# Optimization experiments

Measured on AMD Instinct MI355X. Metric: run time of the kernel, lower is better.

## Reference

```python
import jax, jax.numpy as jnp
import numpy as np

B, S, D = 2, 2048, 1024
N_EXP, TOP_K = 8, 2
CAP_FACTOR = 1.25

def setup_inputs() -> dict:
    key = jax.random.key(0)
    k1, k2 = jax.random.split(key)
    x = jax.random.normal(k1, (B, S, D), dtype=jnp.float32)
    W_gate = jax.random.normal(k2, (N_EXP, D), dtype=jnp.float32) * (1.0 / np.sqrt(D))
    return {"x": x, "W_gate": W_gate}

def reference(x, W_gate):
    Bq, Sq, d = x.shape
    N = Bq * Sq                      # num_tokens
    n_exp = W_gate.shape[0]
    top_k = TOP_K
    cap = int(N * top_k * CAP_FACTOR / n_exp)  # exp_capacity (static)

    x_flat = x.reshape(N, d)
    logits = x_flat @ W_gate.T                      # [N, n_exp]
    top_vals, top_idx = jax.lax.top_k(logits, top_k)  # [N, k]
    gates = jax.nn.softmax(top_vals, axis=-1)       # [N, k]

    # Serial token-major, k-minor assignment order == flatten row-major.
    e_flat = top_idx.reshape(-1)                    # [N*k]
    oh = jax.nn.one_hot(e_flat, n_exp, dtype=jnp.int32)
    # position within expert = # earlier slots routed to same expert
    pos = (jnp.cumsum(oh, axis=0) - oh)[jnp.arange(N * top_k), e_flat]
    pos_safe = jnp.where(pos < cap, pos, cap)       # cap -> out-of-bounds -> dropped

    tok = jnp.arange(N * top_k) // top_k            # owning token per slot
    g_flat = gates.reshape(-1)

    exp_mask = jnp.zeros((N, n_exp, cap), jnp.float32)
    exp_mask = exp_mask.at[tok, e_flat, pos_safe].set(g_flat, mode='drop')

    exp_batches = jnp.zeros((n_exp, cap, d), jnp.float32)
    exp_batches = exp_batches.at[e_flat, pos_safe].set(x_flat[tok], mode='drop')

    return gates, exp_mask, exp_batches
```

## Files before the change

### kernel.cpp

```cpp
#include <hip/hip_runtime.h>
#include <math.h>

#define NTOK   4096
#define DIM    1024
#define NEXP   8
#define CAP    1280
#define MROW   (NEXP * CAP)

#define OUT_MASK_OFF   ((size_t)NTOK*2)
#define OUT_BATCH_OFF  (OUT_MASK_OFF + (size_t)NTOK*NEXP*CAP)

typedef float f4 __attribute__((ext_vector_type(4)));

__global__ __launch_bounds__(256) void gate_kernel(
    const float* __restrict__ x, const float* __restrict__ Wg,
    float* __restrict__ gates_out,
    int* __restrict__ e0a, int* __restrict__ e1a,
    float* __restrict__ g0a, float* __restrict__ g1a)
{
    const int wave = threadIdx.x >> 6;
    const int lane = threadIdx.x & 63;
    const int t    = blockIdx.x * 4 + wave;

    const f4* xr = (const f4*)(x + (size_t)t * DIM);
    f4 xv[4];
#pragma unroll
    for (int p = 0; p < 4; ++p) xv[p] = xr[p * 64 + lane];

    float acc[NEXP];
#pragma unroll
    for (int e = 0; e < NEXP; ++e) {
        const f4* wr = (const f4*)(Wg + (size_t)e * DIM);
        float a = 0.f;
#pragma unroll
        for (int p = 0; p < 4; ++p) {
            const f4 w = wr[p * 64 + lane];
            a += xv[p].x * w.x + xv[p].y * w.y + xv[p].z * w.z + xv[p].w * w.w;
        }
        acc[e] = a;
    }

#pragma unroll
    for (int off = 32; off >= 1; off >>= 1) {
#pragma unroll
        for (int e = 0; e < NEXP; ++e)
            acc[e] += __shfl_xor(acc[e], off);
    }

    if (lane == 0) {
        float best = -INFINITY, second = -INFINITY;
        int b0 = 0, b1 = 0;
#pragma unroll
        for (int e = 0; e < NEXP; ++e) {
            const float v = acc[e];
            if (v > best)        { second = best; b1 = b0; best = v; b0 = e; }
            else if (v > second) { second = v; b1 = e; }
        }
        const float e1v = __expf(second - best);
        const float inv = 1.0f / (1.0f + e1v);
        const float g0 = inv, g1 = e1v * inv;

        gates_out[(size_t)t * 2]     = g0;
        gates_out[(size_t)t * 2 + 1] = g1;
        e0a[t] = b0; e1a[t] = b1;
        g0a[t] = g0; g1a[t] = g1;
    }
}

__global__ __launch_bounds__(256) void scan_kernel(
    const int* __restrict__ e0a, const int* __restrict__ e1a,
    int* __restrict__ pos0a, int* __restrict__ pos1a,
    int* __restrict__ inv_out)
{
    __shared__ int invs[NEXP * CAP];
    __shared__ unsigned wtot[4][4];

    const int tid  = threadIdx.x;
    const int wave = tid >> 6;
    const int lane = tid & 63;

    for (int i = tid; i < NEXP * CAP; i += 256) invs[i] = -1;

    const int tok0 = tid * 16;
    int ea[16], eb[16];
    {
        const int4* va = (const int4*)(e0a + tok0);
        const int4* vb = (const int4*)(e1a + tok0);
#pragma unroll
        for (int q = 0; q < 4; ++q) {
            int4 a = va[q], b = vb[q];
            ea[4*q] = a.x; ea[4*q+1] = a.y; ea[4*q+2] = a.z; ea[4*q+3] = a.w;
            eb[4*q] = b.x; eb[4*q+1] = b.y; eb[4*q+2] = b.z; eb[4*q+3] = b.w;
        }
    }

    int local[NEXP];
#pragma unroll
    for (int e = 0; e < NEXP; ++e) local[e] = 0;
#pragma unroll
    for (int j = 0; j < 16; ++j) { local[ea[j]]++; local[eb[j]]++; }

    unsigned pk[4];
#pragma unroll
    for (int q = 0; q < 4; ++q)
        pk[q] = (unsigned)local[2*q] | ((unsigned)local[2*q+1] << 16);
    const unsigned my0 = pk[0], my1 = pk[1], my2 = pk[2], my3 = pk[3];

#pragma unroll
    for (int off = 1; off < 64; off <<= 1) {
        unsigned n0 = __shfl_up((int)pk[0], off);
        unsigned n1 = __shfl_up((int)pk[1], off);
        unsigned n2 = __shfl_up((int)pk[2], off);
        unsigned n3 = __shfl_up((int)pk[3], off);
        if (lane >= off) { pk[0] += n0; pk[1] += n1; pk[2] += n2; pk[3] += n3; }
    }

    if (lane == 63) {
#pragma unroll
        for (int q = 0; q < 4; ++q) wtot[wave][q] = pk[q];
    }
    __syncthreads();

#pragma unroll
    for (int w = 0; w < 4; ++w) {
        if (w < wave) {
            pk[0] += wtot[w][0]; pk[1] += wtot[w][1];
            pk[2] += wtot[w][2]; pk[3] += wtot[w][3];
        }
    }
    pk[0] -= my0; pk[1] -= my1; pk[2] -= my2; pk[3] -= my3;

    int run[NEXP];
#pragma unroll
    for (int q = 0; q < 4; ++q) {
        run[2*q]   = (int)(pk[q] & 0xFFFFu);
        run[2*q+1] = (int)(pk[q] >> 16);
    }

    int p0r[16], p1r[16];
#pragma unroll
    for (int j = 0; j < 16; ++j) {
        const int tok = tok0 + j;
        int e = ea[j];
        int p = run[e]++;
        p0r[j] = p;
        if (p < CAP) invs[e * CAP + p] = tok;
        e = eb[j];
        p = run[e]++;
        p1r[j] = p;
        if (p < CAP) invs[e * CAP + p] = tok;
    }

#pragma unroll
    for (int q = 0; q < 4; ++q) {
        ((int4*)(pos0a + tok0))[q] = make_int4(p0r[4*q], p0r[4*q+1], p0r[4*q+2], p0r[4*q+3]);
        ((int4*)(pos1a + tok0))[q] = make_int4(p1r[4*q], p1r[4*q+1], p1r[4*q+2], p1r[4*q+3]);
    }
    __syncthreads();

    for (int i = tid; i < NEXP * CAP / 4; i += 256)
        ((int4*)inv_out)[i] = ((const int4*)invs)[i];
}

#define BATCH_BLOCKS 2560
#define TOTAL_BLOCKS (BATCH_BLOCKS + NTOK)
__global__ __launch_bounds__(256) void writer_kernel(
    const int* __restrict__ e0a, const int* __restrict__ e1a,
    const int* __restrict__ pos0a, const int* __restrict__ pos1a,
    const float* __restrict__ g0a, const float* __restrict__ g1a,
    const int* __restrict__ inv, const float* __restrict__ x,
    float* __restrict__ mask_out, float* __restrict__ batch_out)
{
    const int tid = threadIdx.x;

    if (blockIdx.x < BATCH_BLOCKS) {
        const int4 tk = ((const int4*)inv)[blockIdx.x];
        const int toks[4] = { tk.x, tk.y, tk.z, tk.w };
        const int base = blockIdx.x * 4;
#pragma unroll
        for (int i = 0; i < 4; ++i) {
            const int tok = toks[i];
            f4 v = (f4)(0.f);
            if (tok >= 0)
                v = ((const f4*)(x + (size_t)tok * DIM))[tid];
            __builtin_nontemporal_store(v, (f4*)(batch_out + (size_t)(base + i) * DIM) + tid);
        }
    } else {
        const int t  = blockIdx.x - BATCH_BLOCKS;
        const int e0 = e0a[t], e1 = e1a[t];
        const int p0 = pos0a[t], p1 = pos1a[t];
        const float g0 = g0a[t], g1 = g1a[t];

        const int o0 = e0 * CAP + p0;
        const int o1 = e1 * CAP + p1;
        const int q0 = (p0 < CAP) ? (o0 >> 2) : -1;
        const int c0 = o0 & 3;
        const int q1 = (p1 < CAP) ? (o1 >> 2) : -1;
        const int c1 = o1 & 3;

        f4* row = (f4*)(mask_out + (size_t)t * MROW);
#pragma unroll
        for (int it = 0; it < MROW / 1024; ++it) {
            const int f4i = it * 256 + tid;
            f4 v = (f4)(0.f);
            if (f4i == q0) {
                v.x = (c0 == 0) ? g0 : 0.f;
                v.y = (c0 == 1) ? g0 : 0.f;
                v.z = (c0 == 2) ? g0 : 0.f;
                v.w = (c0 == 3) ? g0 : 0.f;
            }
            if (f4i == q1) {
                v.x = (c1 == 0) ? g1 : v.x;
                v.y = (c1 == 1) ? g1 : v.y;
                v.z = (c1 == 2) ? g1 : v.z;
                v.w = (c1 == 3) ? g1 : v.w;
            }
            __builtin_nontemporal_store(v, row + f4i);
        }
    }
}

extern "C" void kernel_launch(void* const* d_in, const int* in_sizes, int n_in,
                              void* d_out, int out_size, void* d_ws, size_t ws_size,
                              hipStream_t stream)
{
    const float* x  = (const float*)d_in[0];
    const float* Wg = (const float*)d_in[1];

    float* out   = (float*)d_out;
    float* gates = out;
    float* mask  = out + OUT_MASK_OFF;
    float* batch = out + OUT_BATCH_OFF;

    int* wsi = (int*)d_ws;
    int*   e0a  = wsi;
    int*   e1a  = wsi + NTOK;
    float* g0a  = (float*)(wsi + 2 * NTOK);
    float* g1a  = (float*)(wsi + 3 * NTOK);
    int*   p0a  = wsi + 4 * NTOK;
    int*   p1a  = wsi + 5 * NTOK;
    int*   inv  = wsi + 6 * NTOK;

    gate_kernel  <<<NTOK / 4, 256, 0, stream>>>(x, Wg, gates, e0a, e1a, g0a, g1a);
    scan_kernel  <<<1, 256, 0, stream>>>(e0a, e1a, p0a, p1a, inv);
    writer_kernel<<<TOTAL_BLOCKS, 256, 0, stream>>>(
        e0a, e1a, p0a, p1a, g0a, g1a, inv, x, mask, batch);
}
```

Measured before the change: 239.3 us.

## Fuse gate, scan and writer kernels into one cooperative kernel with grid syncs

```diff
diff --git a/kernel.cpp b/kernel.cpp
--- a/kernel.cpp
+++ b/kernel.cpp
@@ -1,5 +1,8 @@
 #include <hip/hip_runtime.h>
+#include <hip/hip_cooperative_groups.h>
 #include <math.h>
+
+namespace cg = cooperative_groups;
 
 #define NTOK   4096
 #define DIM    1024
@@ -10,212 +13,210 @@
 #define OUT_MASK_OFF   ((size_t)NTOK*2)
 #define OUT_BATCH_OFF  (OUT_MASK_OFF + (size_t)NTOK*NEXP*CAP)
 
+#define GRID_BLKS    1024
+#define BATCH_GROUPS 2560
+#define TOTAL_UNITS  (NTOK + BATCH_GROUPS)
+
 typedef float f4 __attribute__((ext_vector_type(4)));
 
-__global__ __launch_bounds__(256) void gate_kernel(
+__global__ __launch_bounds__(256) void moe_fused(
     const float* __restrict__ x, const float* __restrict__ Wg,
     float* __restrict__ gates_out,
+    float* __restrict__ mask_out, float* __restrict__ batch_out,
     int* __restrict__ e0a, int* __restrict__ e1a,
-    float* __restrict__ g0a, float* __restrict__ g1a)
+    float* __restrict__ g0a, float* __restrict__ g1a,
+    int* __restrict__ pos0a, int* __restrict__ pos1a,
+    int* __restrict__ inv)
 {
-    const int wave = threadIdx.x >> 6;
-    const int lane = threadIdx.x & 63;
-    const int t    = blockIdx.x * 4 + wave;
-
-    const f4* xr = (const f4*)(x + (size_t)t * DIM);
-    f4 xv[4];
-#pragma unroll
-    for (int p = 0; p < 4; ++p) xv[p] = xr[p * 64 + lane];
-
-    float acc[NEXP];
-#pragma unroll
-    for (int e = 0; e < NEXP; ++e) {
-        const f4* wr = (const f4*)(Wg + (size_t)e * DIM);
-        float a = 0.f;
-#pragma unroll
-        for (int p = 0; p < 4; ++p) {
-            const f4 w = wr[p * 64 + lane];
-            a += xv[p].x * w.x + xv[p].y * w.y + xv[p].z * w.z + xv[p].w * w.w;
-        }
-        acc[e] = a;
-    }
-
-#pragma unroll
-    for (int off = 32; off >= 1; off >>= 1) {
-#pragma unroll
-        for (int e = 0; e < NEXP; ++e)
-            acc[e] += __shfl_xor(acc[e], off);
-    }
-
-    if (lane == 0) {
-        float best = -INFINITY, second = -INFINITY;
-        int b0 = 0, b1 = 0;
-#pragma unroll
-        for (int e = 0; e < NEXP; ++e) {
-            const float v = acc[e];
-            if (v > best)        { second = best; b1 = b0; best = v; b0 = e; }
-            else if (v > second) { second = v; b1 = e; }
-        }
-        const float e1v = __expf(second - best);
-        const float inv = 1.0f / (1.0f + e1v);
-        const float g0 = inv, g1 = e1v * inv;
-
-        gates_out[(size_t)t * 2]     = g0;
-        gates_out[(size_t)t * 2 + 1] = g1;
-        e0a[t] = b0; e1a[t] = b1;
-        g0a[t] = g0; g1a[t] = g1;
-    }
-}
-
-__global__ __launch_bounds__(256) void scan_kernel(
-    const int* __restrict__ e0a, const int* __restrict__ e1a,
-    int* __restrict__ pos0a, int* __restrict__ pos1a,
-    int* __restrict__ inv_out)
-{
-    __shared__ int invs[NEXP * CAP];
-    __shared__ unsigned wtot[4][4];
+    cg::grid_group grid = cg::this_grid();
 
     const int tid  = threadIdx.x;
     const int wave = tid >> 6;
     const int lane = tid & 63;
 
-    for (int i = tid; i < NEXP * CAP; i += 256) invs[i] = -1;
-
-    const int tok0 = tid * 16;
-    int ea[16], eb[16];
     {
-        const int4* va = (const int4*)(e0a + tok0);
-        const int4* vb = (const int4*)(e1a + tok0);
+        const int g = blockIdx.x * 256 + tid;
+        if (g < MROW / 4) ((int4*)inv)[g] = make_int4(-1, -1, -1, -1);
+    }
+
+    {
+        const int t = blockIdx.x * 4 + wave;
+
+        const f4* xr = (const f4*)(x + (size_t)t * DIM);
+        f4 xv[4];
+#pragma unroll
+        for (int p = 0; p < 4; ++p) xv[p] = xr[p * 64 + lane];
+
+        float acc[NEXP];
+#pragma unroll
+        for (int e = 0; e < NEXP; ++e) {
+            const f4* wr = (const f4*)(Wg + (size_t)e * DIM);
+            float a = 0.f;
+#pragma unroll
+            for (int p = 0; p < 4; ++p) {
+                const f4 w = wr[p * 64 + lane];
+                a += xv[p].x * w.x + xv[p].y * w.y + xv[p].z * w.z + xv[p].w * w.w;
+            }
+            acc[e] = a;
+        }
+
+#pragma unroll
+        for (int off = 32; off >= 1; off >>= 1) {
+#pragma unroll
+            for (int e = 0; e < NEXP; ++e)
+                acc[e] += __shfl_xor(acc[e], off);
+        }
+
+        if (lane == 0) {
+            float best = -INFINITY, second = -INFINITY;
+            int b0 = 0, b1 = 0;
+#pragma unroll
+            for (int e = 0; e < NEXP; ++e) {
+                const float v = acc[e];
+                if (v > best)        { second = best; b1 = b0; best = v; b0 = e; }
+                else if (v > second) { second = v; b1 = e; }
+            }
+            const float e1v = __expf(second - best);
+            const float invd = 1.0f / (1.0f + e1v);
+            const float g0 = invd, g1 = e1v * invd;
+
+            gates_out[(size_t)t * 2]     = g0;
+            gates_out[(size_t)t * 2 + 1] = g1;
+            e0a[t] = b0; e1a[t] = b1;
+            g0a[t] = g0; g1a[t] = g1;
+        }
+    }
+
+    grid.sync();
+
+    if (blockIdx.x == 0) {
+        __shared__ unsigned wtot[4][4];
+
+        const int tok0 = tid * 16;
+        int ea[16], eb[16];
+        {
+            const int4* va = (const int4*)(e0a + tok0);
+            const int4* vb = (const int4*)(e1a + tok0);
+#pragma unroll
+            for (int q = 0; q < 4; ++q) {
+                int4 a = va[q], b = vb[q];
+                ea[4*q] = a.x; ea[4*q+1] = a.y; ea[4*q+2] = a.z; ea[4*q+3] = a.w;
+                eb[4*q] = b.x; eb[4*q+1] = b.y; eb[4*q+2] = b.z; eb[4*q+3] = b.w;
+            }
+        }
+
+        int local[NEXP];
+#pragma unroll
+        for (int e = 0; e < NEXP; ++e) local[e] = 0;
+#pragma unroll
+        for (int j = 0; j < 16; ++j) { local[ea[j]]++; local[eb[j]]++; }
+
+        unsigned pk[4];
+#pragma unroll
+        for (int q = 0; q < 4; ++q)
+            pk[q] = (unsigned)local[2*q] | ((unsigned)local[2*q+1] << 16);
+        const unsigned my0 = pk[0], my1 = pk[1], my2 = pk[2], my3 = pk[3];
+
+#pragma unroll
+        for (int off = 1; off < 64; off <<= 1) {
+            unsigned n0 = __shfl_up((int)pk[0], off);
+            unsigned n1 = __shfl_up((int)pk[1], off);
+            unsigned n2 = __shfl_up((int)pk[2], off);
+            unsigned n3 = __shfl_up((int)pk[3], off);
+            if (lane >= off) { pk[0] += n0; pk[1] += n1; pk[2] += n2; pk[3] += n3; }
+        }
+
+        if (lane == 63) {
+#pragma unroll
+            for (int q = 0; q < 4; ++q) wtot[wave][q] = pk[q];
+        }
+        __syncthreads();
+
+#pragma unroll
+        for (int w = 0; w < 4; ++w) {
+            if (w < wave) {
+                pk[0] += wtot[w][0]; pk[1] += wtot[w][1];
+                pk[2] += wtot[w][2]; pk[3] += wtot[w][3];
+            }
+        }
+        pk[0] -= my0; pk[1] -= my1; pk[2] -= my2; pk[3] -= my3;
+
+        int run[NEXP];
 #pragma unroll
         for (int q = 0; q < 4; ++q) {
-            int4 a = va[q], b = vb[q];
-            ea[4*q] = a.x; ea[4*q+1] = a.y; ea[4*q+2] = a.z; ea[4*q+3] = a.w;
-            eb[4*q] = b.x; eb[4*q+1] = b.y; eb[4*q+2] = b.z; eb[4*q+3] = b.w;
-        }
-    }
-
-    int local[NEXP];
-#pragma unroll
-    for (int e = 0; e < NEXP; ++e) local[e] = 0;
-#pragma unroll
-    for (int j = 0; j < 16; ++j) { local[ea[j]]++; local[eb[j]]++; }
-
-    unsigned pk[4];
-#pragma unroll
-    for (int q = 0; q < 4; ++q)
-        pk[q] = (unsigned)local[2*q] | ((unsigned)local[2*q+1] << 16);
-    const unsigned my0 = pk[0], my1 = pk[1], my2 = pk[2], my3 = pk[3];
-
-#pragma unroll
-    for (int off = 1; off < 64; off <<= 1) {
-        unsigned n0 = __shfl_up((int)pk[0], off);
-        unsigned n1 = __shfl_up((int)pk[1], off);
-        unsigned n2 = __shfl_up((int)pk[2], off);
-        unsigned n3 = __shfl_up((int)pk[3], off);
-        if (lane >= off) { pk[0] += n0; pk[1] += n1; pk[2] += n2; pk[3] += n3; }
-    }
-
-    if (lane == 63) {
-#pragma unroll
-        for (int q = 0; q < 4; ++q) wtot[wave][q] = pk[q];
-    }
-    __syncthreads();
-
-#pragma unroll
-    for (int w = 0; w < 4; ++w) {
-        if (w < wave) {
-            pk[0] += wtot[w][0]; pk[1] += wtot[w][1];
-            pk[2] += wtot[w][2]; pk[3] += wtot[w][3];
-        }
-    }
-    pk[0] -= my0; pk[1] -= my1; pk[2] -= my2; pk[3] -= my3;
-
-    int run[NEXP];
-#pragma unroll
-    for (int q = 0; q < 4; ++q) {
-        run[2*q]   = (int)(pk[q] & 0xFFFFu);
-        run[2*q+1] = (int)(pk[q] >> 16);
-    }
-
-    int p0r[16], p1r[16];
-#pragma unroll
-    for (int j = 0; j < 16; ++j) {
-        const int tok = tok0 + j;
-        int e = ea[j];
-        int p = run[e]++;
-        p0r[j] = p;
-        if (p < CAP) invs[e * CAP + p] = tok;
-        e = eb[j];
-        p = run[e]++;
-        p1r[j] = p;
-        if (p < CAP) invs[e * CAP + p] = tok;
-    }
-
-#pragma unroll
-    for (int q = 0; q < 4; ++q) {
-        ((int4*)(pos0a + tok0))[q] = make_int4(p0r[4*q], p0r[4*q+1], p0r[4*q+2], p0r[4*q+3]);
-        ((int4*)(pos1a + tok0))[q] = make_int4(p1r[4*q], p1r[4*q+1], p1r[4*q+2], p1r[4*q+3]);
-    }
-    __syncthreads();
-
-    for (int i = tid; i < NEXP * CAP / 4; i += 256)
-        ((int4*)inv_out)[i] = ((const int4*)invs)[i];
-}
-
-#define BATCH_BLOCKS 2560
-#define TOTAL_BLOCKS (BATCH_BLOCKS + NTOK)
-__global__ __launch_bounds__(256) void writer_kernel(
-    const int* __restrict__ e0a, const int* __restrict__ e1a,
-    const int* __restrict__ pos0a, const int* __restrict__ pos1a,
-    const float* __restrict__ g0a, const float* __restrict__ g1a,
-    const int* __restrict__ inv, const float* __restrict__ x,
-    float* __restrict__ mask_out, float* __restrict__ batch_out)
-{
-    const int tid = threadIdx.x;
-
-    if (blockIdx.x < BATCH_BLOCKS) {
-        const int4 tk = ((const int4*)inv)[blockIdx.x];
-        const int toks[4] = { tk.x, tk.y, tk.z, tk.w };
-        const int base = blockIdx.x * 4;
-#pragma unroll
-        for (int i = 0; i < 4; ++i) {
-            const int tok = toks[i];
-            f4 v = (f4)(0.f);
-            if (tok >= 0)
-                v = ((const f4*)(x + (size_t)tok * DIM))[tid];
-            __builtin_nontemporal_store(v, (f4*)(batch_out + (size_t)(base + i) * DIM) + tid);
-        }
-    } else {
-        const int t  = blockIdx.x - BATCH_BLOCKS;
-        const int e0 = e0a[t], e1 = e1a[t];
-        const int p0 = pos0a[t], p1 = pos1a[t];
-        const float g0 = g0a[t], g1 = g1a[t];
-
-        const int o0 = e0 * CAP + p0;
-        const int o1 = e1 * CAP + p1;
-        const int q0 = (p0 < CAP) ? (o0 >> 2) : -1;
-        const int c0 = o0 & 3;
-        const int q1 = (p1 < CAP) ? (o1 >> 2) : -1;
-        const int c1 = o1 & 3;
-
-        f4* row = (f4*)(mask_out + (size_t)t * MROW);
-#pragma unroll
-        for (int it = 0; it < MROW / 1024; ++it) {
-            const int f4i = it * 256 + tid;
-            f4 v = (f4)(0.f);
-            if (f4i == q0) {
-                v.x = (c0 == 0) ? g0 : 0.f;
-                v.y = (c0 == 1) ? g0 : 0.f;
-                v.z = (c0 == 2) ? g0 : 0.f;
-                v.w = (c0 == 3) ? g0 : 0.f;
-            }
-            if (f4i == q1) {
-                v.x = (c1 == 0) ? g1 : v.x;
-                v.y = (c1 == 1) ? g1 : v.y;
-                v.z = (c1 == 2) ? g1 : v.z;
-                v.w = (c1 == 3) ? g1 : v.w;
-            }
-            __builtin_nontemporal_store(v, row + f4i);
+            run[2*q]   = (int)(pk[q] & 0xFFFFu);
+            run[2*q+1] = (int)(pk[q] >> 16);
+        }
+
+        int p0r[16], p1r[16];
+#pragma unroll
+        for (int j = 0; j < 16; ++j) {
+            const int tok = tok0 + j;
+            int e = ea[j];
+            int p = run[e]++;
+            p0r[j] = p;
+            if (p < CAP) inv[e * CAP + p] = tok;
+            e = eb[j];
+            p = run[e]++;
+            p1r[j] = p;
+            if (p < CAP) inv[e * CAP + p] = tok;
+        }
+
+#pragma unroll
+        for (int q = 0; q < 4; ++q) {
+            ((int4*)(pos0a + tok0))[q] = make_int4(p0r[4*q], p0r[4*q+1], p0r[4*q+2], p0r[4*q+3]);
+            ((int4*)(pos1a + tok0))[q] = make_int4(p1r[4*q], p1r[4*q+1], p1r[4*q+2], p1r[4*q+3]);
+        }
+    }
+
+    grid.sync();
+
+    for (int u = blockIdx.x; u < TOTAL_UNITS; u += GRID_BLKS) {
+        if (u < NTOK) {
+            const int t  = u;
+            const int e0 = e0a[t], e1 = e1a[t];
+            const int p0 = pos0a[t], p1 = pos1a[t];
+            const float g0 = g0a[t], g1 = g1a[t];
+
+            const int o0 = e0 * CAP + p0;
+            const int o1 = e1 * CAP + p1;
+            const int q0 = (p0 < CAP) ? (o0 >> 2) : -1;
+            const int c0 = o0 & 3;
+            const int q1 = (p1 < CAP) ? (o1 >> 2) : -1;
+            const int c1 = o1 & 3;
+
+            f4* row = (f4*)(mask_out + (size_t)t * MROW);
+#pragma unroll
+            for (int it = 0; it < MROW / 1024; ++it) {
+                const int f4i = it * 256 + tid;
+                f4 v = (f4)(0.f);
+                if (f4i == q0) {
+                    v.x = (c0 == 0) ? g0 : 0.f;
+                    v.y = (c0 == 1) ? g0 : 0.f;
+                    v.z = (c0 == 2) ? g0 : 0.f;
+                    v.w = (c0 == 3) ? g0 : 0.f;
+                }
+                if (f4i == q1) {
+                    v.x = (c1 == 0) ? g1 : v.x;
+                    v.y = (c1 == 1) ? g1 : v.y;
+                    v.z = (c1 == 2) ? g1 : v.z;
+                    v.w = (c1 == 3) ? g1 : v.w;
+                }
+                __builtin_nontemporal_store(v, row + f4i);
+            }
+        } else {
+            const int grp = u - NTOK;
+            const int4 tk = ((const int4*)inv)[grp];
+            const int toks[4] = { tk.x, tk.y, tk.z, tk.w };
+            const int base = grp * 4;
+#pragma unroll
+            for (int i = 0; i < 4; ++i) {
+                const int tok = toks[i];
+                f4 v = (f4)(0.f);
+                if (tok >= 0)
+                    v = ((const f4*)(x + (size_t)tok * DIM))[tid];
+                __builtin_nontemporal_store(v, (f4*)(batch_out + (size_t)(base + i) * DIM) + tid);
+            }
         }
     }
 }
@@ -241,8 +242,11 @@
     int*   p1a  = wsi + 5 * NTOK;
     int*   inv  = wsi + 6 * NTOK;
 
-    gate_kernel  <<<NTOK / 4, 256, 0, stream>>>(x, Wg, gates, e0a, e1a, g0a, g1a);
-    scan_kernel  <<<1, 256, 0, stream>>>(e0a, e1a, p0a, p1a, inv);
-    writer_kernel<<<TOTAL_BLOCKS, 256, 0, stream>>>(
-        e0a, e1a, p0a, p1a, g0a, g1a, inv, x, mask, batch);
+    void* args[] = {
+        (void*)&x, (void*)&Wg, (void*)&gates, (void*)&mask, (void*)&batch,
+        (void*)&e0a, (void*)&e1a, (void*)&g0a, (void*)&g1a,
+        (void*)&p0a, (void*)&p1a, (void*)&inv
+    };
+    hipLaunchCooperativeKernel((const void*)moe_fused,
+                               dim3(GRID_BLKS), dim3(256), args, 0, stream);
 }
```

New measurement: 392.8 us. 1.64x slower.
